# Optimization experiments

Measured on AMD Instinct MI355X. Metric: run time of the kernel, lower is better.

The kernel has to match this reference:

```python
import jax, jax.numpy as jnp
import numpy as np

N_NODES = 50000
N_EDGES = 300000
N_CLUSTERS = 100
IN_C = 256
OUT_C = 256


def setup_inputs() -> dict:
    key = jax.random.key(0)
    k1, k2, k3, k4, k5, k6 = jax.random.split(key, 6)
    X = jax.random.normal(k1, (N_NODES, IN_C), dtype=jnp.float32)
    # Cluster-GCN style block partition: contiguous clusters of equal size
    assign = ((jnp.arange(N_NODES) * N_CLUSTERS) // N_NODES).astype(jnp.int32)
    bs = N_NODES // N_CLUSTERS  # block (cluster) size
    src = jax.random.randint(k2, (N_EDGES,), 0, N_NODES)
    intra_dst = (src // bs) * bs + jax.random.randint(k3, (N_EDGES,), 0, bs)
    rand_dst = jax.random.randint(k4, (N_EDGES,), 0, N_NODES)
    dst = jnp.where(jax.random.uniform(k5, (N_EDGES,)) < 0.9, intra_dst, rand_dst)
    full_ei = jnp.stack([src, dst]).astype(jnp.int32)
    W = (jax.random.normal(k6, (IN_C, OUT_C), dtype=jnp.float32) / np.sqrt(IN_C)).astype(jnp.float32)
    b = jnp.zeros((OUT_C,), dtype=jnp.float32)
    return {"X": X, "W": W, "b": b, "assign": assign, "full_ei": full_ei}


def reference(X, W, b, assign, full_ei):
    # Equivalent to the per-cluster loop: GCNConv (add_self_loops=True, symmetric
    # normalization) applied to the subgraph of intra-cluster edges; clusters
    # with zero internal edges are skipped (nodes keep original features).
    N = X.shape[0]
    src, dst = full_ei[0], full_ei[1]
    intra = (assign[src] == assign[dst]).astype(X.dtype)  # [E]
    # per-cluster-subgraph degree, including self loop
    deg = jnp.ones((N,), X.dtype).at[dst].add(intra)  # [N]
    dis = jax.lax.rsqrt(deg)
    xW = X @ W  # [N, out_c]
    w_e = intra * dis[src] * dis[dst]  # [E]
    agg = jax.ops.segment_sum(w_e[:, None] * xW[src], dst, num_segments=N)
    agg = agg + xW / deg[:, None]  # self-loop term: norm = 1/deg
    out = agg + b
    has_edge = jax.ops.segment_sum(intra, assign[src], num_segments=N_CLUSTERS) > 0
    return jnp.where(has_edge[assign][:, None], out, X)
```

## Files before the change

kernel.cpp:

```cpp
#include <hip/hip_runtime.h>
#include <hip/hip_bf16.h>

#define N_NODES 50000
#define N_EDGES 300000
#define N_CLUSTERS 100
#define CH 256
#define CAP 32

typedef __attribute__((ext_vector_type(8))) short short8;
typedef __attribute__((ext_vector_type(4))) float f32x4;

static __device__ inline unsigned short f2bf(float f) {
    unsigned int u = __float_as_uint(f);
    u += 0x7fffu + ((u >> 16) & 1u);
    return (unsigned short)(u >> 16);
}


__global__ void init_kernel(int* __restrict__ indeg, int* __restrict__ flags) {
    int i = blockIdx.x * blockDim.x + threadIdx.x;
    if (i < N_NODES) indeg[i] = 0;
    if (i < N_CLUSTERS) flags[i] = 0;
}

__global__ void scatter_kernel(const int* __restrict__ ei, const int* __restrict__ assign,
                               int* __restrict__ indeg, int* __restrict__ flags,
                               int* __restrict__ csr) {
    int e = blockIdx.x * blockDim.x + threadIdx.x;
    if (e >= N_EDGES) return;
    int s = ei[e], d = ei[N_EDGES + e];
    int cs = assign[s];
    if (cs == assign[d]) {
        int p = atomicAdd(&indeg[d], 1);
        if (p < CAP) csr[d * CAP + p] = s;
        flags[cs] = 1;
    }
}

__global__ void dis_kernel(const int* __restrict__ indeg, float* __restrict__ dis) {
    int i = blockIdx.x * blockDim.x + threadIdx.x;
    if (i < N_NODES) dis[i] = rsqrtf(1.0f + (float)indeg[i]);
}

__global__ void convw_kernel(const float* __restrict__ W, unsigned short* __restrict__ Wt) {
    int n = blockIdx.x, k = threadIdx.x;
    Wt[n * CH + k] = f2bf(W[k * CH + n]);
}


#define BM 128
#define BN 128
#define BK 32
#define LDSS 40

__global__ __launch_bounds__(256) void gemm_bf16(const float* __restrict__ X,
                                                 const unsigned short* __restrict__ Wt,
                                                 unsigned short* __restrict__ xWb) {
    __shared__ unsigned short Xs[BM * LDSS];
    __shared__ unsigned short Ws[BN * LDSS];
    int tid = threadIdx.x;
    int bn = blockIdx.x & 1;
    int bm = blockIdx.x >> 1;
    int row0 = bm * BM, col0 = bn * BN;
    int wid = tid >> 6, lane = tid & 63;
    int wm = (wid & 1) * 64, wn = (wid >> 1) * 64;
    int l15 = lane & 15, quad = lane >> 4;

    f32x4 acc[4][4] = {};

    int srow = tid >> 1;
    int skc  = (tid & 1) * 16;
    int garow = row0 + srow; if (garow >= N_NODES) garow = N_NODES - 1;
    const float*          gA = X  + (size_t)garow * CH + skc;
    const unsigned short* gB = Wt + (size_t)(col0 + srow) * CH + skc;
    unsigned short* lA = &Xs[srow * LDSS + skc];
    unsigned short* lB = &Ws[srow * LDSS + skc];

    for (int k0 = 0; k0 < CH; k0 += BK) {
        float4 x0 = *reinterpret_cast<const float4*>(gA + k0);
        float4 x1 = *reinterpret_cast<const float4*>(gA + k0 + 4);
        float4 x2 = *reinterpret_cast<const float4*>(gA + k0 + 8);
        float4 x3 = *reinterpret_cast<const float4*>(gA + k0 + 12);
        uint4 b0 = *reinterpret_cast<const uint4*>(gB + k0);
        uint4 b1 = *reinterpret_cast<const uint4*>(gB + k0 + 8);
        ushort4 a0 = { f2bf(x0.x), f2bf(x0.y), f2bf(x0.z), f2bf(x0.w) };
        ushort4 a1 = { f2bf(x1.x), f2bf(x1.y), f2bf(x1.z), f2bf(x1.w) };
        ushort4 a2 = { f2bf(x2.x), f2bf(x2.y), f2bf(x2.z), f2bf(x2.w) };
        ushort4 a3 = { f2bf(x3.x), f2bf(x3.y), f2bf(x3.z), f2bf(x3.w) };
        *reinterpret_cast<ushort4*>(lA)      = a0;
        *reinterpret_cast<ushort4*>(lA + 4)  = a1;
        *reinterpret_cast<ushort4*>(lA + 8)  = a2;
        *reinterpret_cast<ushort4*>(lA + 12) = a3;
        *reinterpret_cast<uint4*>(lB)     = b0;
        *reinterpret_cast<uint4*>(lB + 8) = b1;
        __syncthreads();

        short8 af[4], bf[4];
#pragma unroll
        for (int mi = 0; mi < 4; ++mi)
            af[mi] = *reinterpret_cast<const short8*>(&Xs[(wm + mi * 16 + l15) * LDSS + quad * 8]);
#pragma unroll
        for (int ni = 0; ni < 4; ++ni)
            bf[ni] = *reinterpret_cast<const short8*>(&Ws[(wn + ni * 16 + l15) * LDSS + quad * 8]);
#pragma unroll
        for (int mi = 0; mi < 4; ++mi)
#pragma unroll
            for (int ni = 0; ni < 4; ++ni)
                acc[mi][ni] = __builtin_amdgcn_mfma_f32_16x16x32_bf16(af[mi], bf[ni], acc[mi][ni], 0, 0, 0);
        __syncthreads();
    }

#pragma unroll
    for (int mi = 0; mi < 4; ++mi) {
#pragma unroll
        for (int r = 0; r < 4; ++r) {
            int grow = row0 + wm + mi * 16 + quad * 4 + r;
            if (grow < N_NODES) {
                size_t rb = (size_t)grow * CH + col0 + wn + l15;
#pragma unroll
                for (int ni = 0; ni < 4; ++ni)
                    xWb[rb + ni * 16] = f2bf(acc[mi][ni][r]);
            }
        }
    }
}


static __device__ inline void bf4_fma(float w, uint2 v, float& ax, float& ay, float& az, float& aw) {
    ax += w * __uint_as_float(v.x << 16);
    ay += w * __uint_as_float(v.x & 0xffff0000u);
    az += w * __uint_as_float(v.y << 16);
    aw += w * __uint_as_float(v.y & 0xffff0000u);
}

__global__ __launch_bounds__(256) void gather_kernel(const unsigned short* __restrict__ xWb,
        const float* __restrict__ X, const float* __restrict__ b,
        const int* __restrict__ assign, const int* __restrict__ flags,
        const int* __restrict__ indeg, const float* __restrict__ dis,
        const int* __restrict__ csr, float* __restrict__ out) {
    int node = blockIdx.x * 4 + (threadIdx.x >> 6);
    int lane = threadIdx.x & 63;
    if (node >= N_NODES) return;
    float4* out4 = reinterpret_cast<float4*>(out);
    size_t base4 = (size_t)node * 64 + lane;
    if (flags[assign[node]] == 0) {
        out4[base4] = reinterpret_cast<const float4*>(X)[base4];
        return;
    }
    float dn = dis[node];
    int cnt = indeg[node]; if (cnt > CAP) cnt = CAP;

    int   s_l = 0;
    float w_l = 0.0f;
    if (lane < cnt) {
        s_l = csr[node * CAP + lane];
        w_l = dis[s_l] * dn;
    }

    float selfw = dn * dn;
    uint2 sv = *reinterpret_cast<const uint2*>(xWb + (size_t)node * CH + lane * 4);
    float ax = 0, ay = 0, az = 0, aw = 0;
    bf4_fma(selfw, sv, ax, ay, az, aw);

    int i = 0;
    for (; i + 4 <= cnt; i += 4) {
        int   s0 = __shfl(s_l, i),     s1 = __shfl(s_l, i + 1);
        int   s2 = __shfl(s_l, i + 2), s3 = __shfl(s_l, i + 3);
        float w0 = __shfl(w_l, i),     w1 = __shfl(w_l, i + 1);
        float w2 = __shfl(w_l, i + 2), w3 = __shfl(w_l, i + 3);
        uint2 v0 = *reinterpret_cast<const uint2*>(xWb + (size_t)s0 * CH + lane * 4);
        uint2 v1 = *reinterpret_cast<const uint2*>(xWb + (size_t)s1 * CH + lane * 4);
        uint2 v2 = *reinterpret_cast<const uint2*>(xWb + (size_t)s2 * CH + lane * 4);
        uint2 v3 = *reinterpret_cast<const uint2*>(xWb + (size_t)s3 * CH + lane * 4);
        bf4_fma(w0, v0, ax, ay, az, aw);
        bf4_fma(w1, v1, ax, ay, az, aw);
        bf4_fma(w2, v2, ax, ay, az, aw);
        bf4_fma(w3, v3, ax, ay, az, aw);
    }
    for (; i < cnt; ++i) {
        int   s = __shfl(s_l, i);
        float w = __shfl(w_l, i);
        uint2 v = *reinterpret_cast<const uint2*>(xWb + (size_t)s * CH + lane * 4);
        bf4_fma(w, v, ax, ay, az, aw);
    }

    float4 bb = reinterpret_cast<const float4*>(b)[lane];
    float4 o = { ax + bb.x, ay + bb.y, az + bb.z, aw + bb.w };
    out4[base4] = o;
}


extern "C" void kernel_launch(void* const* d_in, const int* in_sizes, int n_in,
                              void* d_out, int out_size, void* d_ws, size_t ws_size,
                              hipStream_t stream) {
    const float* X      = (const float*)d_in[0];
    const float* W      = (const float*)d_in[1];
    const float* b      = (const float*)d_in[2];
    const int*   assign = (const int*)d_in[3];
    const int*   ei     = (const int*)d_in[4];
    float* out = (float*)d_out;

    char* ws = (char*)d_ws;
    size_t off = 0;
    auto alloc = [&](size_t bytes) -> void* {
        void* p = ws + off;
        off = (off + bytes + 255) & ~(size_t)255;
        return p;
    };
    unsigned short* xWb = (unsigned short*)alloc((size_t)N_NODES * CH * sizeof(unsigned short));
    unsigned short* Wt  = (unsigned short*)alloc((size_t)CH * CH * sizeof(unsigned short));
    int*   csr   = (int*)alloc((size_t)N_NODES * CAP * sizeof(int));
    int*   indeg = (int*)alloc(N_NODES * sizeof(int));
    float* dis   = (float*)alloc(N_NODES * sizeof(float));
    int*   flags = (int*)alloc(N_CLUSTERS * sizeof(int));
    (void)ws_size; (void)n_in; (void)in_sizes; (void)out_size;

    init_kernel<<<(N_NODES + 255) / 256, 256, 0, stream>>>(indeg, flags);
    scatter_kernel<<<(N_EDGES + 255) / 256, 256, 0, stream>>>(ei, assign, indeg, flags, csr);
    dis_kernel<<<(N_NODES + 255) / 256, 256, 0, stream>>>(indeg, dis);
    convw_kernel<<<CH, CH, 0, stream>>>(W, Wt);
    gemm_bf16<<<((N_NODES + BM - 1) / BM) * 2, 256, 0, stream>>>(X, Wt, xWb);
    gather_kernel<<<(N_NODES + 3) / 4, 256, 0, stream>>>(xWb, X, b, assign, flags, indeg,
                                                         dis, csr, out);
}
```

Before: 175.5 us.

## Widen GEMM tile to full N, fuse dis into gather, remap gather blocks per XCD

The GEMM now computes all 256 output columns per 128-row block, so each X tile is loaded and converted to bf16 once instead of twice. The cost is a larger accumulator set (128 floats per lane) and more LDS, with a launch_bounds hint of 2 blocks per SU. The dis_kernel launch is removed and rsqrt of the degree is computed inline in the gather. Gather blocks are remapped so consecutive node ranges land on the same XCD, which should improve L2 locality for intra-cluster neighbour reads.

```diff
diff --git a/kernel.cpp b/kernel.cpp
--- a/kernel.cpp
+++ b/kernel.cpp
@@ -37,11 +37,6 @@
     }
 }
 
-__global__ void dis_kernel(const int* __restrict__ indeg, float* __restrict__ dis) {
-    int i = blockIdx.x * blockDim.x + threadIdx.x;
-    if (i < N_NODES) dis[i] = rsqrtf(1.0f + (float)indeg[i]);
-}
-
 __global__ void convw_kernel(const float* __restrict__ W, unsigned short* __restrict__ Wt) {
     int n = blockIdx.x, k = threadIdx.x;
     Wt[n * CH + k] = f2bf(W[k * CH + n]);
@@ -49,32 +44,29 @@
 
 
 #define BM 128
-#define BN 128
 #define BK 32
 #define LDSS 40
 
-__global__ __launch_bounds__(256) void gemm_bf16(const float* __restrict__ X,
-                                                 const unsigned short* __restrict__ Wt,
-                                                 unsigned short* __restrict__ xWb) {
+__global__ __launch_bounds__(256, 2) void gemm_bf16(const float* __restrict__ X,
+                                                    const unsigned short* __restrict__ Wt,
+                                                    unsigned short* __restrict__ xWb) {
     __shared__ unsigned short Xs[BM * LDSS];
-    __shared__ unsigned short Ws[BN * LDSS];
+    __shared__ unsigned short Ws[CH * LDSS];
     int tid = threadIdx.x;
-    int bn = blockIdx.x & 1;
-    int bm = blockIdx.x >> 1;
-    int row0 = bm * BM, col0 = bn * BN;
+    int row0 = blockIdx.x * BM;
     int wid = tid >> 6, lane = tid & 63;
-    int wm = (wid & 1) * 64, wn = (wid >> 1) * 64;
+    int wn = wid * 64;
     int l15 = lane & 15, quad = lane >> 4;
 
-    f32x4 acc[4][4] = {};
+    f32x4 acc[2][4][4] = {};
 
     int srow = tid >> 1;
     int skc  = (tid & 1) * 16;
     int garow = row0 + srow; if (garow >= N_NODES) garow = N_NODES - 1;
-    const float*          gA = X  + (size_t)garow * CH + skc;
-    const unsigned short* gB = Wt + (size_t)(col0 + srow) * CH + skc;
+    const float* gA = X + (size_t)garow * CH + skc;
     unsigned short* lA = &Xs[srow * LDSS + skc];
-    unsigned short* lB = &Ws[srow * LDSS + skc];
+    const unsigned short* gB = Wt + (size_t)tid * CH;
+    unsigned short* lB = &Ws[tid * LDSS];
 
     for (int k0 = 0; k0 < CH; k0 += BK) {
         float4 x0 = *reinterpret_cast<const float4*>(gA + k0);
@@ -83,6 +75,8 @@
         float4 x3 = *reinterpret_cast<const float4*>(gA + k0 + 12);
         uint4 b0 = *reinterpret_cast<const uint4*>(gB + k0);
         uint4 b1 = *reinterpret_cast<const uint4*>(gB + k0 + 8);
+        uint4 b2 = *reinterpret_cast<const uint4*>(gB + k0 + 16);
+        uint4 b3 = *reinterpret_cast<const uint4*>(gB + k0 + 24);
         ushort4 a0 = { f2bf(x0.x), f2bf(x0.y), f2bf(x0.z), f2bf(x0.w) };
         ushort4 a1 = { f2bf(x1.x), f2bf(x1.y), f2bf(x1.z), f2bf(x1.w) };
         ushort4 a2 = { f2bf(x2.x), f2bf(x2.y), f2bf(x2.z), f2bf(x2.w) };
@@ -91,40 +85,53 @@
         *reinterpret_cast<ushort4*>(lA + 4)  = a1;
         *reinterpret_cast<ushort4*>(lA + 8)  = a2;
         *reinterpret_cast<ushort4*>(lA + 12) = a3;
-        *reinterpret_cast<uint4*>(lB)     = b0;
-        *reinterpret_cast<uint4*>(lB + 8) = b1;
+        *reinterpret_cast<uint4*>(lB)      = b0;
+        *reinterpret_cast<uint4*>(lB + 8)  = b1;
+        *reinterpret_cast<uint4*>(lB + 16) = b2;
+        *reinterpret_cast<uint4*>(lB + 24) = b3;
         __syncthreads();
 
-        short8 af[4], bf[4];
+        short8 af[2][4], bf[4];
+#pragma unroll
+        for (int h = 0; h < 2; ++h)
+#pragma unroll
+            for (int mi = 0; mi < 4; ++mi)
+                af[h][mi] = *reinterpret_cast<const short8*>(
+                    &Xs[(h * 64 + mi * 16 + l15) * LDSS + quad * 8]);
+#pragma unroll
+        for (int ni = 0; ni < 4; ++ni)
+            bf[ni] = *reinterpret_cast<const short8*>(
+                &Ws[(wn + ni * 16 + l15) * LDSS + quad * 8]);
+#pragma unroll
+        for (int h = 0; h < 2; ++h)
+#pragma unroll
+            for (int mi = 0; mi < 4; ++mi)
+#pragma unroll
+                for (int ni = 0; ni < 4; ++ni)
+                    acc[h][mi][ni] = __builtin_amdgcn_mfma_f32_16x16x32_bf16(
+                        af[h][mi], bf[ni], acc[h][mi][ni], 0, 0, 0);
+        __syncthreads();
+    }
+
+#pragma unroll
+    for (int h = 0; h < 2; ++h)
 #pragma unroll
         for (int mi = 0; mi < 4; ++mi)
-            af[mi] = *reinterpret_cast<const short8*>(&Xs[(wm + mi * 16 + l15) * LDSS + quad * 8]);
-#pragma unroll
-        for (int ni = 0; ni < 4; ++ni)
-            bf[ni] = *reinterpret_cast<const short8*>(&Ws[(wn + ni * 16 + l15) * LDSS + quad * 8]);
-#pragma unroll
-        for (int mi = 0; mi < 4; ++mi)
-#pragma unroll
-            for (int ni = 0; ni < 4; ++ni)
-                acc[mi][ni] = __builtin_amdgcn_mfma_f32_16x16x32_bf16(af[mi], bf[ni], acc[mi][ni], 0, 0, 0);
-        __syncthreads();
-    }
-
-#pragma unroll
-    for (int mi = 0; mi < 4; ++mi) {
-#pragma unroll
-        for (int r = 0; r < 4; ++r) {
-            int grow = row0 + wm + mi * 16 + quad * 4 + r;
-            if (grow < N_NODES) {
-                size_t rb = (size_t)grow * CH + col0 + wn + l15;
-#pragma unroll
-                for (int ni = 0; ni < 4; ++ni)
-                    xWb[rb + ni * 16] = f2bf(acc[mi][ni][r]);
+#pragma unroll
+            for (int r = 0; r < 4; ++r) {
+                int grow = row0 + h * 64 + mi * 16 + quad * 4 + r;
+                if (grow < N_NODES) {
+                    size_t rb = (size_t)grow * CH + wn + l15;
+#pragma unroll
+                    for (int ni = 0; ni < 4; ++ni)
+                        xWb[rb + ni * 16] = f2bf(acc[h][mi][ni][r]);
+                }
             }
-        }
-    }
-}
-
+}
+
+
+#define NBLK ((N_NODES + 3) / 4)
+#define BLK_PER_XCD ((NBLK + 7) / 8)
 
 static __device__ inline void bf4_fma(float w, uint2 v, float& ax, float& ay, float& az, float& aw) {
     ax += w * __uint_as_float(v.x << 16);
@@ -136,9 +143,11 @@
 __global__ __launch_bounds__(256) void gather_kernel(const unsigned short* __restrict__ xWb,
         const float* __restrict__ X, const float* __restrict__ b,
         const int* __restrict__ assign, const int* __restrict__ flags,
-        const int* __restrict__ indeg, const float* __restrict__ dis,
-        const int* __restrict__ csr, float* __restrict__ out) {
-    int node = blockIdx.x * 4 + (threadIdx.x >> 6);
+        const int* __restrict__ indeg, const int* __restrict__ csr,
+        float* __restrict__ out) {
+    int blk = (blockIdx.x & 7) * BLK_PER_XCD + (blockIdx.x >> 3);
+    if (blk >= NBLK) return;
+    int node = blk * 4 + (threadIdx.x >> 6);
     int lane = threadIdx.x & 63;
     if (node >= N_NODES) return;
     float4* out4 = reinterpret_cast<float4*>(out);
@@ -147,14 +156,15 @@
         out4[base4] = reinterpret_cast<const float4*>(X)[base4];
         return;
     }
-    float dn = dis[node];
-    int cnt = indeg[node]; if (cnt > CAP) cnt = CAP;
+    int cnt_raw = indeg[node];
+    int cnt = cnt_raw > CAP ? CAP : cnt_raw;
+    float dn = rsqrtf(1.0f + (float)cnt_raw);
 
     int   s_l = 0;
     float w_l = 0.0f;
     if (lane < cnt) {
         s_l = csr[node * CAP + lane];
-        w_l = dis[s_l] * dn;
+        w_l = rsqrtf(1.0f + (float)indeg[s_l]) * dn;
     }
 
     float selfw = dn * dn;
@@ -211,15 +221,13 @@
     unsigned short* Wt  = (unsigned short*)alloc((size_t)CH * CH * sizeof(unsigned short));
     int*   csr   = (int*)alloc((size_t)N_NODES * CAP * sizeof(int));
     int*   indeg = (int*)alloc(N_NODES * sizeof(int));
-    float* dis   = (float*)alloc(N_NODES * sizeof(float));
     int*   flags = (int*)alloc(N_CLUSTERS * sizeof(int));
     (void)ws_size; (void)n_in; (void)in_sizes; (void)out_size;
 
     init_kernel<<<(N_NODES + 255) / 256, 256, 0, stream>>>(indeg, flags);
     scatter_kernel<<<(N_EDGES + 255) / 256, 256, 0, stream>>>(ei, assign, indeg, flags, csr);
-    dis_kernel<<<(N_NODES + 255) / 256, 256, 0, stream>>>(indeg, dis);
     convw_kernel<<<CH, CH, 0, stream>>>(W, Wt);
-    gemm_bf16<<<((N_NODES + BM - 1) / BM) * 2, 256, 0, stream>>>(X, Wt, xWb);
-    gather_kernel<<<(N_NODES + 3) / 4, 256, 0, stream>>>(xWb, X, b, assign, flags, indeg,
-                                                         dis, csr, out);
-}
+    gemm_bf16<<<(N_NODES + BM - 1) / BM, 256, 0, stream>>>(X, Wt, xWb);
+    gather_kernel<<<BLK_PER_XCD * 8, 256, 0, stream>>>(xWb, X, b, assign, flags, indeg,
+                                                       csr, out);
+}
```

New measurement: 181.5 us. 3.4% more time.
